# Kernel optimization log

Measured on AMD Instinct MI355X. Metric: run time of the kernel, lower is better.

The kernel has to match this reference:

```python
import jax, jax.numpy as jnp
import numpy as np

N_HEADS = 16
HEAD = 64
SEQ = 2048
EMBED = 1024
BATCH = 4

def setup_inputs() -> dict:
    key = jax.random.key(0)
    ks = jax.random.split(key, 6)
    inputs = jax.random.normal(ks[0], (BATCH, SEQ, EMBED), dtype=jnp.float32)
    # per-head projection weights stacked: [H, E, D] (nn.Linear(E, D, bias=False))
    s = 1.0 / np.sqrt(EMBED)
    Wq = jax.random.uniform(ks[1], (N_HEADS, EMBED, HEAD), jnp.float32, -s, s)
    Wk = jax.random.uniform(ks[2], (N_HEADS, EMBED, HEAD), jnp.float32, -s, s)
    Wv = jax.random.uniform(ks[3], (N_HEADS, EMBED, HEAD), jnp.float32, -s, s)
    Wo = jax.random.uniform(ks[4], (EMBED, EMBED), jnp.float32, -s, s)
    bo = jax.random.uniform(ks[5], (EMBED,), jnp.float32, -s, s)
    return {"inputs": inputs, "Wq": Wq, "Wk": Wk, "Wv": Wv, "Wo": Wo, "bo": bo}

def reference(inputs, Wq, Wk, Wv, Wo, bo):
    B, S, E = inputs.shape
    # batched per-head projections: [B,S,E] x [H,E,D] -> [B,H,S,D]
    q = jnp.einsum('bse,hed->bhsd', inputs, Wq)
    k = jnp.einsum('bse,hed->bhsd', inputs, Wk)
    v = jnp.einsum('bse,hed->bhsd', inputs, Wv)
    q = q / jnp.sqrt(jnp.float32(HEAD)).astype(q.dtype)
    scores = jnp.einsum('bhsd,bhtd->bhst', q, k)  # [B,H,S,S]
    causal = jnp.tril(jnp.ones((S, S), dtype=bool))
    scores = jnp.where(causal, scores, jnp.finfo(scores.dtype).min)
    weights = jax.nn.softmax(scores, axis=-1)
    out = jnp.einsum('bhst,bhtd->bhsd', weights, v)  # [B,H,S,D]
    # concat heads in head order -> [B,S,H*D]
    out = jnp.transpose(out, (0, 2, 1, 3)).reshape(B, S, N_HEADS * HEAD)
    return out @ Wo.T + bo
```

## Files before the change

kernel.cpp:

```cpp
#include <hip/hip_runtime.h>
#include <stdint.h>

typedef unsigned short ushort_t;
typedef __attribute__((ext_vector_type(8))) short short8;
typedef __attribute__((ext_vector_type(4))) short bf16x4;
typedef __attribute__((ext_vector_type(4))) float f32x4;

#define AS1 __attribute__((address_space(1)))
#define AS3 __attribute__((address_space(3)))

__device__ __forceinline__ void gl_lds16(const void* g, void* l) {
    __builtin_amdgcn_global_load_lds((const AS1 unsigned int*)g,
                                     (AS3 unsigned int*)l, 16, 0, 0);
}

__device__ __forceinline__ ushort_t f2bf(float f) {
    union { float f; unsigned u; } v; v.f = f;
    unsigned r = v.u + 0x7fffu + ((v.u >> 16) & 1u);
    return (ushort_t)(r >> 16);
}

__global__ __launch_bounds__(256) void prep_k(const float* __restrict__ inp,
                                              const float* __restrict__ Wo,
                                              const float* __restrict__ Wq,
                                              const float* __restrict__ Wk,
                                              const float* __restrict__ Wv,
                                              ushort_t* __restrict__ inp_bf,
                                              ushort_t* __restrict__ WoB,
                                              ushort_t* __restrict__ WT) {
    const int bx = blockIdx.x, tid = threadIdx.x;
    if (bx < 4608) {
        const float* src = (bx < 4096) ? inp : Wo;
        ushort_t* dst    = (bx < 4096) ? inp_bf : WoB;
        int i = ((bx < 4096 ? bx : bx - 4096) * 256 + tid) * 8;
        float4 a = *(const float4*)(src + i);
        float4 b = *(const float4*)(src + i + 4);
        short8 o;
        o[0] = (short)f2bf(a.x); o[1] = (short)f2bf(a.y);
        o[2] = (short)f2bf(a.z); o[3] = (short)f2bf(a.w);
        o[4] = (short)f2bf(b.x); o[5] = (short)f2bf(b.y);
        o[6] = (short)f2bf(b.z); o[7] = (short)f2bf(b.w);
        *(short8*)(dst + i) = o;
        return;
    }
    __shared__ ushort_t t[64 * 65];
    const int wb = bx - 4608;
    const int mat = wb >> 8;
    const int h   = (wb >> 4) & 15;
    const int et  = wb & 15;
    const float* W = (mat == 0 ? Wq : (mat == 1 ? Wk : Wv)) + h * (1024 * 64);
    const float* src = W + et * 64 * 64;
#pragma unroll
    for (int i = 0; i < 16; ++i) {
        int idx = i * 256 + tid;
        int e = idx >> 6, d = idx & 63;
        t[e * 65 + d] = f2bf(src[idx]);
    }
    __syncthreads();
    ushort_t* dst = WT + (mat * 16 + h) * (64 * 1024) + et * 64;
#pragma unroll
    for (int i = 0; i < 16; ++i) {
        int idx = i * 256 + tid;
        int d = idx >> 6, e = idx & 63;
        dst[d * 1024 + e] = t[e * 65 + d];
    }
}

__global__ __launch_bounds__(512, 2) void qkv_k(const ushort_t* __restrict__ A,
                                                const ushort_t* __restrict__ WT,
                                                ushort_t* __restrict__ Q,
                                                ushort_t* __restrict__ K,
                                                ushort_t* __restrict__ Vt) {
    __shared__ __align__(16) ushort_t ring[49152];
    const int tid = threadIdx.x, wave = tid >> 6, lane = tid & 63;
    const int ln15 = lane & 15, quad = lane >> 4;
    const int wm = wave >> 1, wn = wave & 1;
    const int m0 = blockIdx.x * 256, n0 = blockIdx.y * 128;

    const int sa_row  = wave * 16 + (lane >> 2);
    const int sa_colS = (((lane & 3) ^ ((lane >> 3) & 3))) * 8;
    const int woff    = wave * 512;
    const int rchunk  = (quad ^ ((ln15 >> 1) & 3)) * 8;

    f32x4 acc[4][4];
#pragma unroll
    for (int i = 0; i < 4; ++i)
#pragma unroll
        for (int j = 0; j < 4; ++j)
#pragma unroll
            for (int e = 0; e < 4; ++e) acc[i][j][e] = 0.f;

    auto stage = [&](int t) {
        const int kb = t * 32;
        ushort_t* buf = &ring[(t & 3) * 12288];
        gl_lds16(A  + (size_t)(m0 + sa_row)       * 1024 + kb + sa_colS, buf + woff);
        gl_lds16(A  + (size_t)(m0 + 128 + sa_row) * 1024 + kb + sa_colS, buf + 4096 + woff);
        gl_lds16(WT + (size_t)(n0 + sa_row)       * 1024 + kb + sa_colS, buf + 8192 + woff);
    };

    stage(0); stage(1); stage(2);
    asm volatile("s_waitcnt vmcnt(6)" ::: "memory");
    __builtin_amdgcn_s_barrier();
    __builtin_amdgcn_sched_barrier(0);

    for (int t = 0; t < 32; ++t) {
        const ushort_t* buf = &ring[(t & 3) * 12288];
        short8 a[4], b[4];
#pragma unroll
        for (int f = 0; f < 4; ++f)
            a[f] = *(const short8*)&buf[(wm * 64 + f * 16 + ln15) * 32 + rchunk];
#pragma unroll
        for (int f = 0; f < 4; ++f)
            b[f] = *(const short8*)&buf[8192 + (wn * 64 + f * 16 + ln15) * 32 + rchunk];
        if (t + 3 < 32) stage(t + 3);
        if (t < 29)       asm volatile("s_waitcnt vmcnt(6)" ::: "memory");
        else if (t == 29) asm volatile("s_waitcnt vmcnt(3)" ::: "memory");
        else if (t == 30) asm volatile("s_waitcnt vmcnt(0)" ::: "memory");
        __builtin_amdgcn_s_setprio(1);
#pragma unroll
        for (int fm = 0; fm < 4; ++fm)
#pragma unroll
            for (int fn = 0; fn < 4; ++fn)
                acc[fm][fn] = __builtin_amdgcn_mfma_f32_16x16x32_bf16(a[fm], b[fn], acc[fm][fn], 0, 0, 0);
        __builtin_amdgcn_s_setprio(0);
        __builtin_amdgcn_s_barrier();
        __builtin_amdgcn_sched_barrier(0);
    }

    const int n_base = n0 + wn * 64;
    const int mat = n_base >> 10;
    const int h   = (n_base >> 6) & 15;
    if (mat < 2) {
        ushort_t* dst = (mat == 0) ? Q : K;
        const float scale = (mat == 0) ? 0.125f : 1.0f;
#pragma unroll
        for (int fm = 0; fm < 4; ++fm) {
#pragma unroll
            for (int r = 0; r < 4; ++r) {
                int mg = m0 + wm * 64 + fm * 16 + quad * 4 + r;
                int bi = mg >> 11, s = mg & 2047;
                size_t base = ((size_t)(bi * 16 + h) * 2048 + s) * 64;
#pragma unroll
                for (int fn = 0; fn < 4; ++fn)
                    dst[base + fn * 16 + ln15] = f2bf(acc[fm][fn][r] * scale);
            }
        }
    } else {
        ushort_t* tb = &ring[wave * 6144];
#pragma unroll
        for (int fn = 0; fn < 4; ++fn)
#pragma unroll
            for (int fm = 0; fm < 4; ++fm) {
                bf16x4 pk;
#pragma unroll
                for (int r = 0; r < 4; ++r) pk[r] = (short)f2bf(acc[fm][fn][r]);
                *(bf16x4*)&tb[(fn * 16 + ln15) * 72 + fm * 16 + quad * 4] = pk;
            }
        const int s0 = m0 + wm * 64;
        const int bi = s0 >> 11, sb = s0 & 2047;
#pragma unroll
        for (int p = 0; p < 8; ++p) {
            int d  = p * 8 + (lane >> 3);
            int sc = (lane & 7) * 8;
            short8 vv = *(const short8*)&tb[d * 72 + sc];
            *(short8*)&Vt[((size_t)(bi * 16 + h) * 64 + d) * 2048 + sb + sc] = vv;
        }
    }
}

__global__ __launch_bounds__(256, 3) void flash_k(const ushort_t* Q, const ushort_t* K,
                                                  const ushort_t* Vt, ushort_t* Aout) {
    __shared__ __align__(16) ushort_t Ks[2][64 * 64];
    __shared__ __align__(16) ushort_t Vts[2][64 * 64];
    __shared__ __align__(16) ushort_t PT[4][32 * 72];
    const int tid = threadIdx.x, wave = tid >> 6, lane = tid & 63;
    const int ln15 = lane & 15, quad = lane >> 4;
    const int bx = blockIdx.x;
    const int qt = 15 - (bx >> 6);
    const int bh = bx & 63;
    const int qw = qt * 128 + wave * 32;
    const ushort_t* Kb = K + (size_t)bh * 2048 * 64;
    const ushort_t* Vb = Vt + (size_t)bh * 64 * 2048;
    ushort_t* myPT = PT[wave];
    const int srow = tid >> 3, c8 = (tid & 7) * 8;
    const int c8s  = ((tid & 7) ^ ((tid >> 3) & 7)) * 8;
    const int swr  = ln15 & 7;

    short8 qf[2][2];
    {
        const ushort_t* Qb = Q + (size_t)bh * 2048 * 64;
#pragma unroll
        for (int qs = 0; qs < 2; ++qs)
#pragma unroll
            for (int kk = 0; kk < 2; ++kk)
                qf[qs][kk] = *(const short8*)&Qb[(size_t)(qw + qs * 16 + ln15) * 64 + kk * 32 + quad * 8];
    }

    f32x4 o[4][2];
#pragma unroll
    for (int dt = 0; dt < 4; ++dt)
#pragma unroll
        for (int qs = 0; qs < 2; ++qs)
#pragma unroll
            for (int e = 0; e < 4; ++e) o[dt][qs][e] = 0.f;
    float l_s[2] = {0.f, 0.f};

    const int ktEnd = 2 * qt + 2;
    gl_lds16(Kb + (size_t)srow * 64 + c8s,        &Ks[0][srow * 64 + c8]);
    gl_lds16(Kb + (size_t)(32 + srow) * 64 + c8s, &Ks[0][(32 + srow) * 64 + c8]);
    gl_lds16(Vb + (size_t)srow * 2048 + c8s,        &Vts[0][srow * 64 + c8]);
    gl_lds16(Vb + (size_t)(32 + srow) * 2048 + c8s, &Vts[0][(32 + srow) * 64 + c8]);
    __syncthreads();

    for (int kt = 0; kt < ktEnd; ++kt) {
        const int cur = kt & 1, nxt = cur ^ 1;
        if (kt + 1 < ktEnd) {
            int kn = kt + 1;
            gl_lds16(Kb + (size_t)(kn * 64 + srow) * 64 + c8s,      &Ks[nxt][srow * 64 + c8]);
            gl_lds16(Kb + (size_t)(kn * 64 + 32 + srow) * 64 + c8s, &Ks[nxt][(32 + srow) * 64 + c8]);
            gl_lds16(Vb + (size_t)srow * 2048 + kn * 64 + c8s,        &Vts[nxt][srow * 64 + c8]);
            gl_lds16(Vb + (size_t)(32 + srow) * 2048 + kn * 64 + c8s, &Vts[nxt][(32 + srow) * 64 + c8]);
        }
        if (kt * 64 <= qw + 31) {
            f32x4 sc[4][2];
#pragma unroll
            for (int ks = 0; ks < 4; ++ks) {
#pragma unroll
                for (int qs = 0; qs < 2; ++qs)
#pragma unroll
                    for (int e = 0; e < 4; ++e) sc[ks][qs][e] = 0.f;
#pragma unroll
                for (int kk = 0; kk < 2; ++kk) {
                    short8 kf = *(const short8*)&Ks[cur][(ks * 16 + ln15) * 64 + ((kk * 4 + quad) ^ swr) * 8];
#pragma unroll
                    for (int qs = 0; qs < 2; ++qs)
                        sc[ks][qs] = __builtin_amdgcn_mfma_f32_16x16x32_bf16(kf, qf[qs][kk], sc[ks][qs], 0, 0, 0);
                }
            }
            if (kt * 64 + 63 > qw) {
#pragma unroll
                for (int ks = 0; ks < 4; ++ks)
#pragma unroll
                    for (int qs = 0; qs < 2; ++qs) {
                        int qg = qw + qs * 16 + ln15;
#pragma unroll
                        for (int r = 0; r < 4; ++r) {
                            int kg = kt * 64 + ks * 16 + quad * 4 + r;
                            if (kg > qg) sc[ks][qs][r] = -1e30f;
                        }
                    }
            }
#pragma unroll
            for (int qs = 0; qs < 2; ++qs) {
#pragma unroll
                for (int ks = 0; ks < 4; ++ks) {
                    bf16x4 pk;
#pragma unroll
                    for (int r = 0; r < 4; ++r) {
                        float p = __expf(sc[ks][qs][r]);
                        l_s[qs] += p;
                        pk[r] = (short)f2bf(p);
                    }
                    *(bf16x4*)&myPT[(qs * 16 + ln15) * 72 + ks * 16 + quad * 4] = pk;
                }
            }
            short8 pf[2][2];
#pragma unroll
            for (int qs = 0; qs < 2; ++qs)
#pragma unroll
                for (int kk = 0; kk < 2; ++kk)
                    pf[qs][kk] = *(const short8*)&myPT[(qs * 16 + ln15) * 72 + kk * 32 + quad * 8];
#pragma unroll
            for (int dt = 0; dt < 4; ++dt)
#pragma unroll
                for (int kk = 0; kk < 2; ++kk) {
                    short8 vf = *(const short8*)&Vts[cur][(dt * 16 + ln15) * 64 + ((kk * 4 + quad) ^ swr) * 8];
#pragma unroll
                    for (int qs = 0; qs < 2; ++qs)
                        o[dt][qs] = __builtin_amdgcn_mfma_f32_16x16x32_bf16(vf, pf[qs][kk], o[dt][qs], 0, 0, 0);
                }
        }
        __syncthreads();
    }
#pragma unroll
    for (int qs = 0; qs < 2; ++qs) {
        float l = l_s[qs];
        l += __shfl_xor(l, 16);
        l += __shfl_xor(l, 32);
        float inv = 1.f / l;
#pragma unroll
        for (int dt = 0; dt < 4; ++dt) {
            bf16x4 pk;
#pragma unroll
            for (int r = 0; r < 4; ++r) pk[r] = (short)f2bf(o[dt][qs][r] * inv);
            *(bf16x4*)&myPT[(qs * 16 + ln15) * 72 + dt * 16 + quad * 4] = pk;
        }
    }
    const int bi = bh >> 4, h = bh & 15;
#pragma unroll
    for (int p = 0; p < 4; ++p) {
        int row = p * 8 + (lane >> 3);
        int cc = (lane & 7) * 8;
        short8 vv = *(const short8*)&myPT[row * 72 + cc];
        int qg = qw + row;
        *(short8*)&Aout[((size_t)bi * 2048 + qg) * 1024 + h * 64 + cc] = vv;
    }
}

__global__ __launch_bounds__(256) void outproj_k(const ushort_t* A, const ushort_t* WoB,
                                                 const float* bo, float* Out) {
    __shared__ __align__(16) ushort_t As[2][128 * 64];
    __shared__ __align__(16) ushort_t Bs[2][128 * 64];
    const int tid = threadIdx.x, wave = tid >> 6, lane = tid & 63;
    const int ln15 = lane & 15, quad = lane >> 4;
    const int wm = wave >> 1, wn = wave & 1;
    const int lrow = lane >> 3, lcol = (lane & 7) * 8;
    const int lcolS = ((lane & 7) ^ (lane >> 3)) * 8;
    const int swr   = ln15 & 7;
    const int m0 = blockIdx.x * 128, n0 = blockIdx.y * 128;

    f32x4 acc[4][4];
#pragma unroll
    for (int i = 0; i < 4; ++i)
#pragma unroll
        for (int j = 0; j < 4; ++j)
#pragma unroll
            for (int e = 0; e < 4; ++e) acc[i][j][e] = 0.f;

#pragma unroll
    for (int i = 0; i < 4; ++i) {
        int br = i * 32 + wave * 8;
        gl_lds16(A   + (size_t)(m0 + br + lrow) * 1024 + lcolS, &As[0][br * 64]);
        gl_lds16(WoB + (size_t)(n0 + br + lrow) * 1024 + lcolS, &Bs[0][br * 64]);
    }
    __syncthreads();

    for (int it = 0; it < 16; ++it) {
        const int cur = it & 1, nxt = cur ^ 1;
        if (it < 15) {
            const int k0 = (it + 1) * 64;
#pragma unroll
            for (int i = 0; i < 4; ++i) {
                int br = i * 32 + wave * 8;
                gl_lds16(A   + (size_t)(m0 + br + lrow) * 1024 + k0 + lcolS, &As[nxt][br * 64]);
                gl_lds16(WoB + (size_t)(n0 + br + lrow) * 1024 + k0 + lcolS, &Bs[nxt][br * 64]);
            }
        }
#pragma unroll
        for (int kk = 0; kk < 2; ++kk) {
            short8 a[4], b[4];
#pragma unroll
            for (int f = 0; f < 4; ++f)
                a[f] = *(const short8*)&As[cur][(wm * 64 + f * 16 + ln15) * 64 + ((kk * 4 + quad) ^ swr) * 8];
#pragma unroll
            for (int f = 0; f < 4; ++f)
                b[f] = *(const short8*)&Bs[cur][(wn * 64 + f * 16 + ln15) * 64 + ((kk * 4 + quad) ^ swr) * 8];
#pragma unroll
            for (int fm = 0; fm < 4; ++fm)
#pragma unroll
                for (int fn = 0; fn < 4; ++fn)
                    acc[fm][fn] = __builtin_amdgcn_mfma_f32_16x16x32_bf16(a[fm], b[fn], acc[fm][fn], 0, 0, 0);
        }
        __syncthreads();
    }
#pragma unroll
    for (int fn = 0; fn < 4; ++fn) {
        int n = n0 + wn * 64 + fn * 16 + ln15;
        float bias = bo[n];
#pragma unroll
        for (int fm = 0; fm < 4; ++fm)
#pragma unroll
            for (int r = 0; r < 4; ++r) {
                int mg = m0 + wm * 64 + fm * 16 + quad * 4 + r;
                Out[(size_t)mg * 1024 + n] = acc[fm][fn][r] + bias;
            }
    }
}

extern "C" void kernel_launch(void* const* d_in, const int* in_sizes, int n_in,
                              void* d_out, int out_size, void* d_ws, size_t ws_size,
                              hipStream_t stream) {
    (void)in_sizes; (void)n_in; (void)out_size; (void)ws_size;
    const float* inp = (const float*)d_in[0];
    const float* Wq  = (const float*)d_in[1];
    const float* Wk  = (const float*)d_in[2];
    const float* Wv  = (const float*)d_in[3];
    const float* Wo  = (const float*)d_in[4];
    const float* bo  = (const float*)d_in[5];
    float* out = (float*)d_out;

    ushort_t* ws = (ushort_t*)d_ws;
    ushort_t* R0  = ws;
    ushort_t* WT  = R0  + 8388608;
    ushort_t* WoB = WT  + 3145728;
    ushort_t* Qb  = WoB + 1048576;
    ushort_t* Kb  = Qb  + 8388608;
    ushort_t* Vtb = Kb  + 8388608;

    ushort_t* inp_bf = R0;
    ushort_t* At     = R0;

    prep_k<<<5376, 256, 0, stream>>>(inp, Wo, Wq, Wk, Wv, inp_bf, WoB, WT);
    qkv_k<<<dim3(32, 24), 512, 0, stream>>>(inp_bf, WT, Qb, Kb, Vtb);
    flash_k<<<dim3(1024), 256, 0, stream>>>(Qb, Kb, Vtb, At);
    outproj_k<<<dim3(64, 8), 256, 0, stream>>>(At, WoB, bo, out);
}
```

Before: 234.7 us.

## Shrink QKV GEMM LDS ring to three stages for higher occupancy; prioritize attention MFMAs

The QKV projection GEMM drops from a 4-deep to a 3-deep LDS staging ring, which reduces shared memory per block. It raises the launch-bounds occupancy target from 2 to 4 blocks of 512 threads. The main loop is unrolled by three with fixed buffer pointers, so the modulo indexing goes away, and the prefetch distance falls from 3 to 2 tiles. The attention kernel also wraps its QK and PV MFMA blocks in s_setprio. The higher occupancy target may force register spilling given the 64-float accumulator per thread, and the shorter prefetch distance exposes more memory latency.

```diff
diff --git a/kernel.cpp b/kernel.cpp
--- a/kernel.cpp
+++ b/kernel.cpp
@@ -66,12 +66,12 @@
     }
 }
 
-__global__ __launch_bounds__(512, 2) void qkv_k(const ushort_t* __restrict__ A,
+__global__ __launch_bounds__(512, 4) void qkv_k(const ushort_t* __restrict__ A,
                                                 const ushort_t* __restrict__ WT,
                                                 ushort_t* __restrict__ Q,
                                                 ushort_t* __restrict__ K,
                                                 ushort_t* __restrict__ Vt) {
-    __shared__ __align__(16) ushort_t ring[49152];
+    __shared__ __align__(16) ushort_t ring[36864];
     const int tid = threadIdx.x, wave = tid >> 6, lane = tid & 63;
     const int ln15 = lane & 15, quad = lane >> 4;
     const int wm = wave >> 1, wn = wave & 1;
@@ -90,32 +90,30 @@
 #pragma unroll
             for (int e = 0; e < 4; ++e) acc[i][j][e] = 0.f;
 
-    auto stage = [&](int t) {
+    auto stage = [&](int t, ushort_t* buf) {
         const int kb = t * 32;
-        ushort_t* buf = &ring[(t & 3) * 12288];
         gl_lds16(A  + (size_t)(m0 + sa_row)       * 1024 + kb + sa_colS, buf + woff);
         gl_lds16(A  + (size_t)(m0 + 128 + sa_row) * 1024 + kb + sa_colS, buf + 4096 + woff);
         gl_lds16(WT + (size_t)(n0 + sa_row)       * 1024 + kb + sa_colS, buf + 8192 + woff);
     };
 
-    stage(0); stage(1); stage(2);
-    asm volatile("s_waitcnt vmcnt(6)" ::: "memory");
+    stage(0, &ring[0]); stage(1, &ring[12288]);
+    asm volatile("s_waitcnt vmcnt(3)" ::: "memory");
     __builtin_amdgcn_s_barrier();
     __builtin_amdgcn_sched_barrier(0);
 
-    for (int t = 0; t < 32; ++t) {
-        const ushort_t* buf = &ring[(t & 3) * 12288];
+    auto phase = [&](int t, const ushort_t* bufC, ushort_t* bufS) {
         short8 a[4], b[4];
 #pragma unroll
         for (int f = 0; f < 4; ++f)
-            a[f] = *(const short8*)&buf[(wm * 64 + f * 16 + ln15) * 32 + rchunk];
+            a[f] = *(const short8*)&bufC[(wm * 64 + f * 16 + ln15) * 32 + rchunk];
 #pragma unroll
         for (int f = 0; f < 4; ++f)
-            b[f] = *(const short8*)&buf[8192 + (wn * 64 + f * 16 + ln15) * 32 + rchunk];
-        if (t + 3 < 32) stage(t + 3);
-        if (t < 29)       asm volatile("s_waitcnt vmcnt(6)" ::: "memory");
-        else if (t == 29) asm volatile("s_waitcnt vmcnt(3)" ::: "memory");
+            b[f] = *(const short8*)&bufC[8192 + (wn * 64 + f * 16 + ln15) * 32 + rchunk];
+        if (t + 2 < 32) stage(t + 2, bufS);
+        if (t < 30)       asm volatile("s_waitcnt vmcnt(3)" ::: "memory");
         else if (t == 30) asm volatile("s_waitcnt vmcnt(0)" ::: "memory");
+        __builtin_amdgcn_sched_barrier(0);
         __builtin_amdgcn_s_setprio(1);
 #pragma unroll
         for (int fm = 0; fm < 4; ++fm)
@@ -125,7 +123,15 @@
         __builtin_amdgcn_s_setprio(0);
         __builtin_amdgcn_s_barrier();
         __builtin_amdgcn_sched_barrier(0);
-    }
+    };
+
+    for (int t3 = 0; t3 < 30; t3 += 3) {
+        phase(t3,     &ring[0],     &ring[24576]);
+        phase(t3 + 1, &ring[12288], &ring[0]);
+        phase(t3 + 2, &ring[24576], &ring[12288]);
+    }
+    phase(30, &ring[0],     &ring[24576]);
+    phase(31, &ring[12288], &ring[0]);
 
     const int n_base = n0 + wn * 64;
     const int mat = n_base >> 10;
@@ -146,7 +152,7 @@
             }
         }
     } else {
-        ushort_t* tb = &ring[wave * 6144];
+        ushort_t* tb = &ring[wave * 4608];
 #pragma unroll
         for (int fn = 0; fn < 4; ++fn)
 #pragma unroll
@@ -229,6 +235,10 @@
                 for (int qs = 0; qs < 2; ++qs)
 #pragma unroll
                     for (int e = 0; e < 4; ++e) sc[ks][qs][e] = 0.f;
+            }
+            __builtin_amdgcn_s_setprio(1);
+#pragma unroll
+            for (int ks = 0; ks < 4; ++ks) {
 #pragma unroll
                 for (int kk = 0; kk < 2; ++kk) {
                     short8 kf = *(const short8*)&Ks[cur][(ks * 16 + ln15) * 64 + ((kk * 4 + quad) ^ swr) * 8];
@@ -237,6 +247,7 @@
                         sc[ks][qs] = __builtin_amdgcn_mfma_f32_16x16x32_bf16(kf, qf[qs][kk], sc[ks][qs], 0, 0, 0);
                 }
             }
+            __builtin_amdgcn_s_setprio(0);
             if (kt * 64 + 63 > qw) {
 #pragma unroll
                 for (int ks = 0; ks < 4; ++ks)
@@ -270,6 +281,7 @@
 #pragma unroll
                 for (int kk = 0; kk < 2; ++kk)
                     pf[qs][kk] = *(const short8*)&myPT[(qs * 16 + ln15) * 72 + kk * 32 + quad * 8];
+            __builtin_amdgcn_s_setprio(1);
 #pragma unroll
             for (int dt = 0; dt < 4; ++dt)
 #pragma unroll
@@ -279,6 +291,7 @@
                     for (int qs = 0; qs < 2; ++qs)
                         o[dt][qs] = __builtin_amdgcn_mfma_f32_16x16x32_bf16(vf, pf[qs][kk], o[dt][qs], 0, 0, 0);
                 }
+            __builtin_amdgcn_s_setprio(0);
         }
         __syncthreads();
     }
```

Result: faster. 226.1 us (-3.7%).
